# Kernel tuning notes

Hardware: AMD Instinct MI355X
Metric: run time of the kernel (lower is better)

Reference implementation:

```python
import jax, jax.numpy as jnp
import numpy as np

V, E, H, S, B, T = 32000, 256, 512, 128, 32, 32


def setup_inputs() -> dict:
    key = jax.random.key(0)
    ks = iter(jax.random.split(key, 32))

    def w(shape, s=0.05):
        return jax.random.normal(next(ks), shape, dtype=jnp.float32) * s

    return dict(
        src=jax.random.randint(next(ks), (S, B), 0, V),
        trg=jax.random.randint(next(ks), (T, B), 0, V),
        embed=w((V, E)),
        enc_Wih_f=w((4 * H, E)), enc_Whh_f=w((4 * H, H)), enc_bih_f=w((4 * H,)), enc_bhh_f=w((4 * H,)),
        enc_Wih_b=w((4 * H, E)), enc_Whh_b=w((4 * H, H)), enc_bih_b=w((4 * H,)), enc_bhh_b=w((4 * H,)),
        attn_W=w((H, 2 * H)), attn_b=w((H,)), attn_v=w((H,)),
        dec_Wih0=w((4 * H, H + E)), dec_Whh0=w((4 * H, H)), dec_bih0=w((4 * H,)), dec_bhh0=w((4 * H,)),
        dec_Wih1=w((4 * H, H)), dec_Whh1=w((4 * H, H)), dec_bih1=w((4 * H,)), dec_bhh1=w((4 * H,)),
        out_W=w((V, 2 * H)), out_b=w((V,)),
    )


def _cell(x, h, c, Wih, Whh, bih, bhh):
    # PyTorch LSTM gate order: i, f, g, o
    z = x @ Wih.T + h @ Whh.T + bih + bhh
    i, f, g, o = jnp.split(z, 4, axis=-1)
    c2 = jax.nn.sigmoid(f) * c + jax.nn.sigmoid(i) * jnp.tanh(g)
    h2 = jax.nn.sigmoid(o) * jnp.tanh(c2)
    return h2, c2


def _run_lstm(xs, Wih, Whh, bih, bhh):
    # xs: [S, B, in]; returns outputs [S,B,H], final (h,c)
    h0 = jnp.zeros((xs.shape[1], Whh.shape[1]), xs.dtype)

    def step(carry, x):
        h, c = carry
        h2, c2 = _cell(x, h, c, Wih, Whh, bih, bhh)
        return (h2, c2), h2

    (hT, cT), outs = jax.lax.scan(step, (h0, h0), xs)
    return outs, hT, cT


def _forward(src, trg, embed,
             enc_Wih_f, enc_Whh_f, enc_bih_f, enc_bhh_f,
             enc_Wih_b, enc_Whh_b, enc_bih_b, enc_bhh_b,
             attn_W, attn_b, attn_v,
             dec_Wih0, dec_Whh0, dec_bih0, dec_bhh0,
             dec_Wih1, dec_Whh1, dec_bih1, dec_bhh1,
             out_W, out_b):
    emb_src = embed[src]                                  # [S,B,E]
    # bidirectional 1-layer encoder LSTM
    f_outs, hf, cf = _run_lstm(emb_src, enc_Wih_f, enc_Whh_f, enc_bih_f, enc_bhh_f)
    b_outs, hb, cb = _run_lstm(emb_src[::-1], enc_Wih_b, enc_Whh_b, enc_bih_b, enc_bhh_b)
    enc_out = f_outs + b_outs[::-1]                       # [S,B,H] (sum of directions)
    h = jnp.stack([hf, hb])                               # [2,B,H] -> decoder init state
    c = jnp.stack([cf, cb])
    enc_bsh = enc_out.transpose(1, 0, 2)                  # [B,S,H]

    def dec_step(carry, tok):
        h, c = carry
        emb = embed[tok]                                  # [B,E]
        q = h[-1]                                         # top-layer hidden [B,H]
        qs = jnp.broadcast_to(q[:, None, :], enc_bsh.shape)
        energy = jnp.tanh(jnp.concatenate([qs, enc_bsh], -1) @ attn_W.T + attn_b)  # [B,S,H]
        scores = energy @ attn_v                          # [B,S]
        aw = jax.nn.softmax(scores, axis=1)
        ctx = jnp.einsum('bs,bsh->bh', aw, enc_bsh)       # [B,H]
        x = jnp.concatenate([emb, ctx], -1)               # [B,E+H]
        h0, c0 = _cell(x, h[0], c[0], dec_Wih0, dec_Whh0, dec_bih0, dec_bhh0)
        h1, c1 = _cell(h0, h[1], c[1], dec_Wih1, dec_Whh1, dec_bih1, dec_bhh1)
        logits = jax.nn.log_softmax(
            jnp.concatenate([h1, ctx], -1) @ out_W.T + out_b, axis=-1)             # [B,V]
        return (jnp.stack([h0, h1]), jnp.stack([c0, c1])), logits

    # teacher forcing (ratio=1.0): input at step t is trg[t-1]
    _, outs = jax.lax.scan(dec_step, (h, c), trg[:-1])    # [T-1,B,V]
    outputs = jnp.concatenate(
        [jnp.zeros((1,) + outs.shape[1:], outs.dtype), outs], 0)  # outputs[0]=0 as in torch
    return outputs


def reference(src, trg, embed,
              enc_Wih_f, enc_Whh_f, enc_bih_f, enc_bhh_f,
              enc_Wih_b, enc_Whh_b, enc_bih_b, enc_bhh_b,
              attn_W, attn_b, attn_v,
              dec_Wih0, dec_Whh0, dec_bih0, dec_bhh0,
              dec_Wih1, dec_Whh1, dec_bih1, dec_bhh1,
              out_W, out_b):
    return _forward(src, trg, embed,
                    enc_Wih_f, enc_Whh_f, enc_bih_f, enc_bhh_f,
                    enc_Wih_b, enc_Whh_b, enc_bih_b, enc_bhh_b,
                    attn_W, attn_b, attn_v,
                    dec_Wih0, dec_Whh0, dec_bih0, dec_bhh0,
                    dec_Wih1, dec_Whh1, dec_bih1, dec_bhh1,
                    out_W, out_b)
```

## Files before the change

### kernel.cpp

```cpp
#include <hip/hip_runtime.h>
#include <stdint.h>


using short8 = __attribute__((ext_vector_type(8))) short;
using f32x4  = __attribute__((ext_vector_type(4))) float;
typedef _Float16 half2v __attribute__((ext_vector_type(2)));

__device__ __forceinline__ short f2bf(float x){
  unsigned u = __float_as_uint(x);
  unsigned r = (u + 0x7fffu + ((u >> 16) & 1u)) >> 16;
  return (short)(unsigned short)r;
}
__device__ __forceinline__ float bf2f_lo(unsigned u){ return __uint_as_float(u << 16); }
__device__ __forceinline__ float bf2f_hi(unsigned u){ return __uint_as_float(u & 0xffff0000u); }
__device__ __forceinline__ float sigmf(float x){ return 1.0f/(1.0f + __expf(-x)); }
__device__ __forceinline__ float fast_tanh(float x){
  const float e = __expf(2.0f*x);
  return 1.0f - 2.0f/(e + 1.0f);
}
__device__ __forceinline__ unsigned pack_h2(float a, float b){
  unsigned short ha = __builtin_bit_cast(unsigned short, (_Float16)a);
  unsigned short hb = __builtin_bit_cast(unsigned short, (_Float16)b);
  return (unsigned)ha | ((unsigned)hb << 16);
}
__device__ __forceinline__ float dot2u(unsigned x, unsigned w, float c){
#if __has_builtin(__builtin_amdgcn_fdot2)
  return __builtin_amdgcn_fdot2(__builtin_bit_cast(half2v,x), __builtin_bit_cast(half2v,w), c, false);
#else
  half2v hx = __builtin_bit_cast(half2v,x), hw = __builtin_bit_cast(half2v,w);
  c = fmaf((float)hx[0], (float)hw[0], c);
  c = fmaf((float)hx[1], (float)hw[1], c);
  return c;
#endif
}

__device__ __forceinline__ float4 load_coh_f4(const float* p){
  float4 v;
  asm volatile("global_load_dwordx4 %0, %1, off sc0 sc1\n\ts_waitcnt vmcnt(0)"
               : "=&v"(v) : "v"(p) : "memory");
  return v;
}
__device__ __forceinline__ uint4 load_coh_u4(const unsigned* p){
  uint4 v;
  asm volatile("global_load_dwordx4 %0, %1, off sc0 sc1\n\ts_waitcnt vmcnt(0)"
               : "=&v"(v) : "v"(p) : "memory");
  return v;
}
__device__ __forceinline__ void load_coh_f4x4(const float* p0, const float* p1,
                                              const float* p2, const float* p3, float4* d){
  asm volatile(
    "global_load_dwordx4 %0, %4, off sc0 sc1\n\t"
    "global_load_dwordx4 %1, %5, off sc0 sc1\n\t"
    "global_load_dwordx4 %2, %6, off sc0 sc1\n\t"
    "global_load_dwordx4 %3, %7, off sc0 sc1\n\t"
    "s_waitcnt vmcnt(0)"
    : "=&v"(d[0]),"=&v"(d[1]),"=&v"(d[2]),"=&v"(d[3])
    : "v"(p0),"v"(p1),"v"(p2),"v"(p3)
    : "memory");
}
__device__ __forceinline__ void store_coh_f32(float* p, float v){
  asm volatile("global_store_dword %0, %1, off sc0 sc1" :: "v"(p), "v"(v) : "memory");
}
__device__ __forceinline__ void store_coh_u32(unsigned* p, unsigned v){
  asm volatile("global_store_dword %0, %1, off sc0 sc1" :: "v"(p), "v"(v) : "memory");
}

__device__ __forceinline__ void wait_flags(const unsigned* base, int quads, unsigned target){
  if (threadIdx.x < 64){
    const unsigned* p = base + ((threadIdx.x & (quads-1)) << 2);
    for(;;){
      uint4 v = load_coh_u4(p);
      if (__all(v.x>=target && v.y>=target && v.z>=target && v.w>=target)) break;
    }
  }
  __syncthreads();
}
__device__ __forceinline__ void set_flag(unsigned* slot, unsigned val){
  asm volatile("s_waitcnt vmcnt(0)" ::: "memory");
  __syncthreads();
  if (threadIdx.x == 0) store_coh_u32(slot, val);
}

__device__ __forceinline__ void stage8b(const float* src, unsigned* lds, int ldl){
  const int tid = threadIdx.x;
  const int row0 = tid >> 7;
  const int k4 = tid & 127;
  const float* p0 = src + (size_t)(row0    )*512 + (k4<<2);
  const float* p1 = src + (size_t)(row0 + 2)*512 + (k4<<2);
  const float* p2 = src + (size_t)(row0 + 4)*512 + (k4<<2);
  const float* p3 = src + (size_t)(row0 + 6)*512 + (k4<<2);
  float4 v[4];
  load_coh_f4x4(p0, p1, p2, p3, v);
  #pragma unroll
  for (int i = 0; i < 4; ++i){
    const int row = row0 + 2*i;
    lds[row*ldl + (k4<<1)]     = pack_h2(v[i].x, v[i].y);
    lds[row*ldl + (k4<<1) + 1] = pack_h2(v[i].z, v[i].w);
  }
}

__device__ __forceinline__ float dot512(const unsigned* xrow, const unsigned* w){
  float a = 0.f;
  #pragma unroll 4
  for (int it = 0; it < 16; ++it){
    uint4 x0 = *(const uint4*)(xrow + it*16);
    uint4 x1 = *(const uint4*)(xrow + it*16 + 4);
    uint4 x2 = *(const uint4*)(xrow + it*16 + 8);
    uint4 x3 = *(const uint4*)(xrow + it*16 + 12);
    uint4 w0 = *(const uint4*)(w + it*16);
    uint4 w1 = *(const uint4*)(w + it*16 + 4);
    uint4 w2 = *(const uint4*)(w + it*16 + 8);
    uint4 w3 = *(const uint4*)(w + it*16 + 12);
    a = dot2u(x0.x,w0.x,a); a = dot2u(x0.y,w0.y,a); a = dot2u(x0.z,w0.z,a); a = dot2u(x0.w,w0.w,a);
    a = dot2u(x1.x,w1.x,a); a = dot2u(x1.y,w1.y,a); a = dot2u(x1.z,w1.z,a); a = dot2u(x1.w,w1.w,a);
    a = dot2u(x2.x,w2.x,a); a = dot2u(x2.y,w2.y,a); a = dot2u(x2.z,w2.z,a); a = dot2u(x2.w,w2.w,a);
    a = dot2u(x3.x,w3.x,a); a = dot2u(x3.y,w3.y,a); a = dot2u(x3.z,w3.z,a); a = dot2u(x3.w,w3.w,a);
  }
  return a;
}

__device__ __forceinline__ float2 dot2rows(const unsigned* xrow, const unsigned* wA, const unsigned* wB){
  float a = 0.f, b = 0.f;
  #pragma unroll 8
  for (int it = 0; it < 32; ++it){
    uint4 x0 = *(const uint4*)(xrow + it*8);
    uint4 x1 = *(const uint4*)(xrow + it*8 + 4);
    uint4 a0 = *(const uint4*)(wA + it*8);
    uint4 a1 = *(const uint4*)(wA + it*8 + 4);
    uint4 b0 = *(const uint4*)(wB + it*8);
    uint4 b1 = *(const uint4*)(wB + it*8 + 4);
    a = dot2u(x0.x,a0.x,a); a = dot2u(x0.y,a0.y,a); a = dot2u(x0.z,a0.z,a); a = dot2u(x0.w,a0.w,a);
    a = dot2u(x1.x,a1.x,a); a = dot2u(x1.y,a1.y,a); a = dot2u(x1.z,a1.z,a); a = dot2u(x1.w,a1.w,a);
    b = dot2u(x0.x,b0.x,b); b = dot2u(x0.y,b0.y,b); b = dot2u(x0.z,b0.z,b); b = dot2u(x0.w,b0.w,b);
    b = dot2u(x1.x,b1.x,b); b = dot2u(x1.y,b1.y,b); b = dot2u(x1.w,b1.w,b); b = dot2u(x1.z,b1.z,b);
  }
  return make_float2(a, b);
}

__global__ void k_zero(float* __restrict__ p, int n){
  int i = blockIdx.x*256 + threadIdx.x;
  const int stride = gridDim.x*256;
  for (; i < n; i += stride) p[i] = 0.f;
}

__global__ __launch_bounds__(256) void k_cvt_f16(const float* __restrict__ s, unsigned short* __restrict__ d, int n){
  int i = blockIdx.x*256 + threadIdx.x;
  const int stride = gridDim.x*256;
  for (; i < n; i += stride) d[i] = __builtin_bit_cast(unsigned short, (_Float16)s[i]);
}
__global__ __launch_bounds__(256) void k_cvt_f16_str(const float* __restrict__ s, int lds_, unsigned short* __restrict__ d, int n){
  int i = blockIdx.x*256 + threadIdx.x;
  const int stride = gridDim.x*256;
  for (; i < n; i += stride){
    const int row = i >> 9, c = i & 511;
    d[i] = __builtin_bit_cast(unsigned short, (_Float16)s[(size_t)row*lds_ + c]);
  }
}

__global__ __launch_bounds__(256) void k_gather(
    const int* __restrict__ src, const int* __restrict__ trg,
    const float* __restrict__ embed,
    short* __restrict__ emb_src_bf, short* __restrict__ emb_trg_bf)
{
  const int row = blockIdx.x, tid = threadIdx.x;
  if (row < 4096){
    const int tok = src[row];
    emb_src_bf[(size_t)row*256 + tid] = f2bf(embed[(size_t)tok*256 + tid]);
  } else {
    const int r = row - 4096;
    short v = 0;
    if (r < 992){ const int tok = trg[r]; v = f2bf(embed[(size_t)tok*256 + tid]); }
    emb_trg_bf[(size_t)r*256 + tid] = v;
  }
}

__global__ __launch_bounds__(256) void k_gemm_aw(
    const short* __restrict__ A, int lda,
    const float* __restrict__ W, int ldw,
    float* __restrict__ C, int ldc,
    const float* __restrict__ bias0, const float* __restrict__ bias1,
    int Mvalid, int K, int tmode, short* __restrict__ Cbf)
{
  __shared__ __align__(16) short As[128*32];
  __shared__ __align__(16) short Bs[128*32];
  const int tid = threadIdx.x;
  const int bm = blockIdx.x, bn = blockIdx.y;
  const int w  = tid >> 6,  l  = tid & 63;
  const int wm = w >> 1,    wn = w & 1;
  const int lr = l & 15,    lk = l >> 4;

  const int r0 = tid >> 2;
  const int s0 = (tid & 3) << 3;
  const int r1 = r0 + 64;

  const short* a0 = A + (size_t)(bm*128 + r0)*lda + s0;
  const short* a1 = A + (size_t)(bm*128 + r1)*lda + s0;
  const float* w0 = W + (size_t)(bn*128 + r0)*ldw + s0;
  const float* w1 = W + (size_t)(bn*128 + r1)*ldw + s0;

  const f32x4 zero4 = {0.f,0.f,0.f,0.f};
  f32x4 acc[4][4];
  #pragma unroll
  for (int mi=0;mi<4;mi++){
    #pragma unroll
    for (int ni=0;ni<4;ni++) acc[mi][ni] = zero4;
  }

  for (int k0 = 0; k0 < K; k0 += 32){
    short8 va0 = *(const short8*)(a0 + k0);
    short8 va1 = *(const short8*)(a1 + k0);
    float4 f00 = *(const float4*)(w0 + k0);
    float4 f01 = *(const float4*)(w0 + k0 + 4);
    float4 f10 = *(const float4*)(w1 + k0);
    float4 f11 = *(const float4*)(w1 + k0 + 4);
    short8 vb0, vb1;
    vb0[0]=f2bf(f00.x); vb0[1]=f2bf(f00.y); vb0[2]=f2bf(f00.z); vb0[3]=f2bf(f00.w);
    vb0[4]=f2bf(f01.x); vb0[5]=f2bf(f01.y); vb0[6]=f2bf(f01.z); vb0[7]=f2bf(f01.w);
    vb1[0]=f2bf(f10.x); vb1[1]=f2bf(f10.y); vb1[2]=f2bf(f10.z); vb1[3]=f2bf(f10.w);
    vb1[4]=f2bf(f11.x); vb1[5]=f2bf(f11.y); vb1[6]=f2bf(f11.z); vb1[7]=f2bf(f11.w);

    __syncthreads();
    *((short8*)As + tid)       = va0;
    *((short8*)As + tid + 256) = va1;
    *((short8*)Bs + tid)       = vb0;
    *((short8*)Bs + tid + 256) = vb1;
    __syncthreads();

    short8 af[4], bfr[4];
    #pragma unroll
    for (int mi=0;mi<4;mi++) af[mi]  = *(const short8*)&As[(wm*64 + mi*16 + lr)*32 + (lk<<3)];
    #pragma unroll
    for (int ni=0;ni<4;ni++) bfr[ni] = *(const short8*)&Bs[(wn*64 + ni*16 + lr)*32 + (lk<<3)];
    #pragma unroll
    for (int mi=0;mi<4;mi++){
      #pragma unroll
      for (int ni=0;ni<4;ni++)
        acc[mi][ni] = __builtin_amdgcn_mfma_f32_16x16x32_bf16(af[mi], bfr[ni], acc[mi][ni], 0,0,0);
    }
  }

  #pragma unroll
  for (int mi=0;mi<4;mi++){
    const int rb = bm*128 + wm*64 + mi*16 + (lk<<2);
    #pragma unroll
    for (int ni=0;ni<4;ni++){
      const int col = bn*128 + wn*64 + ni*16 + lr;
      float bv = 0.f;
      if (bias0) bv += bias0[col];
      if (bias1) bv += bias1[col];
      #pragma unroll
      for (int rr=0;rr<4;rr++){
        const int row = rb + rr;
        if (row < Mvalid){
          const float vv = acc[mi][ni][rr] + bv;
          if (Cbf)        Cbf[(size_t)row*ldc + col] = f2bf(vv);
          else if (tmode) C[(size_t)(row>>5)*65536 + (size_t)col*32 + (row&31)] = vv;
          else            C[(size_t)row*ldc + col] = vv;
        }
      }
    }
  }
}

__global__ __launch_bounds__(256,1) void k_enc_persist(
    const float* __restrict__ pre_f, const float* __restrict__ pre_b,
    const unsigned short* __restrict__ WhF, const unsigned short* __restrict__ WhB,
    float* __restrict__ f_outs, float* __restrict__ b_outs,
    float* __restrict__ c_f_out, float* __restrict__ c_b_out,
    unsigned* __restrict__ flagF, unsigned* __restrict__ flagB)
{
  __shared__ __align__(16) unsigned x_lds[8*264];
  __shared__ float zbuf[64*8];
  const int bid = blockIdx.x, tid = threadIdx.x;
  const int x = bid & 7, m = bid >> 3;
  const int dir = m & 1, bg = (m >> 1) & 3, q = m >> 3;
  const int jb = x*4 + q;
  const float* pre = dir ? pre_b : pre_f;
  const unsigned* Wh = (const unsigned*)(dir ? WhB : WhF);
  float* outs = dir ? b_outs : f_outs;
  float* c_out = dir ? c_b_out : c_f_out;
  unsigned* flags = dir ? flagB : flagF;
  const int fid = jb + 32*bg;

  const int bb = tid & 7, rr = tid >> 3;
  const int g = rr >> 3, op = rr & 7;
  const unsigned* wA = Wh + (size_t)(g*512 + jb*16 + 2*op)*256;
  const unsigned* wB = wA + 256;

  const int fo = tid & 15, fb = tid >> 4;
  const int b_out = bg*8 + fb, k_out = jb*16 + fo;
  float c_reg = 0.f;

  for (int t = 0; t < 128; ++t){
    float pz[4];
    if (tid < 128){
      const int tt = dir ? (127 - t) : t;
      const float* pt = pre + (size_t)tt*65536;
      #pragma unroll
      for (int gg = 0; gg < 4; ++gg)
        pz[gg] = pt[(size_t)(gg*512 + k_out)*32 + b_out];
    }
    if (t) wait_flags(flags + 32*bg, 8, (unsigned)t);
    if (t == 0){
      for (int i = tid; i < 8*264; i += 256) x_lds[i] = 0;
    } else {
      stage8b(outs + (size_t)(t-1)*16384 + (size_t)(bg*8)*512, x_lds, 264);
    }
    __syncthreads();

    const float2 d = dot2rows(x_lds + bb*264, wA, wB);
    zbuf[(g*16 + 2*op)*8 + bb]   = d.x;
    zbuf[(g*16 + 2*op+1)*8 + bb] = d.y;
    __syncthreads();

    if (tid < 128){
      float z[4];
      #pragma unroll
      for (int gg = 0; gg < 4; ++gg)
        z[gg] = pz[gg] + zbuf[(gg*16 + fo)*8 + fb];
      const float cn = sigmf(z[1])*c_reg + sigmf(z[0])*fast_tanh(z[2]);
      c_reg = cn;
      store_coh_f32(outs + (size_t)t*16384 + (size_t)b_out*512 + k_out, sigmf(z[3])*fast_tanh(cn));
    }
    set_flag(flags + fid, (unsigned)(t+1));
  }
  if (tid < 128) c_out[b_out*512 + k_out] = c_reg;
}

__global__ __launch_bounds__(256) void k_sum_enc(
    const float* __restrict__ f_outs, const float* __restrict__ b_outs,
    short* __restrict__ enc_sum_bf)
{
  const int i = blockIdx.x*256 + threadIdx.x;
  const int s = i >> 14, rem = i & 16383;
  enc_sum_bf[i] = f2bf(f_outs[i] + b_outs[(size_t)(127 - s)*16384 + rem]);
}

__global__ __launch_bounds__(256,1) void k_dec_persist(
    const float* __restrict__ demb,
    const unsigned short* __restrict__ Wih0h,
    const unsigned short* __restrict__ Whh0h,
    const unsigned short* __restrict__ Wih1h,
    const unsigned short* __restrict__ Whh1h,
    const float* __restrict__ bih1, const float* __restrict__ bhh1,
    const unsigned short* __restrict__ wqh,
    const float* __restrict__ attnV,
    const short* __restrict__ enc_proj_bf,
    const short* __restrict__ enc_sum_bf,
    const float* __restrict__ h0_init, const float* __restrict__ h1_init,
    const float* __restrict__ c0_init, const float* __restrict__ c1_init,
    float* __restrict__ h0buf, float* __restrict__ h1buf,
    float* __restrict__ ctxb,
    float* __restrict__ qsb,
    short* __restrict__ h1ctx,
    unsigned* __restrict__ dflag)
{
  __shared__ __align__(16) unsigned x0s[8*260];
  __shared__ __align__(16) unsigned x1s[8*260];
  __shared__ float zfin[32*9];
  __shared__ __align__(16) float q_s[512], v_s[512];
  __shared__ float part[256], aw[128], red[128];

  const int bid = blockIdx.x, tid = threadIdx.x;
  const int jb = (bid & 7)*8 + ((bid >> 3) >> 2);
  const int bg = (bid >> 3) & 3;
  const int fid = bg*64 + jb;
  unsigned* gq = dflag + bg*64;

  const int b = tid & 7, r = tid >> 3;
  const int g = r >> 3, o = r & 7;
  const int j_row = g*512 + jb*8 + o;

  const int fo = tid & 7, fb = tid >> 3;
  const int b_out = bg*8 + fb, k_out = jb*8 + fo;

  const unsigned* Wh0row = (const unsigned*)Whh0h + (size_t)j_row*256;
  const unsigned* Wh1row = (const unsigned*)Whh1h + (size_t)j_row*256;
  const unsigned* Wi0row = (const unsigned*)Wih0h + (size_t)j_row*256;
  const unsigned* Wi1row = (const unsigned*)Wih1h + (size_t)j_row*256;
  const unsigned* Wqrow  = (const unsigned*)wqh  + (size_t)(jb*8 + b)*256;

  float c0_reg = 0.f, c1_reg = 0.f, bias1g[4];
  if (tid < 64){
    c0_reg = c0_init[b_out*512 + k_out];
    c1_reg = c1_init[b_out*512 + k_out];
    #pragma unroll
    for (int gg=0; gg<4; ++gg) bias1g[gg] = bih1[gg*512 + k_out] + bhh1[gg*512 + k_out];
  }
  if (bid < 32 && tid < 128) ((float4*)v_s)[tid] = ((const float4*)attnV)[tid];

  float zh0 = 0.f;

  for (int t = 0; t < 31; ++t){
    const float demb_v = demb[(size_t)t*65536 + (size_t)j_row*32 + bg*8 + b];

    if (t){
      wait_flags(gq, 16, (unsigned)(4*t));
      stage8b(h1buf + (size_t)(t&1)*16384 + (size_t)(bg*8)*512, x1s, 260);
    } else {
      stage8b(h0_init + (size_t)(bg*8)*512, x0s, 260);
      stage8b(h1_init + (size_t)(bg*8)*512, x1s, 260);
    }
    __syncthreads();
    if (t == 0) zh0 = dot512(x0s + b*260, Wh0row);
    const float zh1 = dot512(x1s + b*260, Wh1row);
    if (tid < 64){
      const float qv = dot512(x1s + (tid>>3)*260, Wqrow);
      store_coh_f32(qsb + (size_t)(bg*8 + (tid>>3))*512 + jb*8 + b, qv);
    }

    if (bid < 32){
      set_flag(dflag + fid, (unsigned)(4*t+1));
      wait_flags(gq, 16, (unsigned)(4*t+1));
      const int ab = bid;
      if (tid < 128) ((float4*)q_s)[tid] = load_coh_f4(qsb + (size_t)ab*512 + (tid<<2));
      __syncthreads();
      {
        const int s = tid >> 1, half = tid & 1;
        const unsigned* ep = (const unsigned*)(enc_proj_bf + ((size_t)(s*32 + ab))*512 + (half << 8));
        const float* qh = q_s + (half << 8);
        const float* vh = v_s + (half << 8);
        float p = 0.f;
        for (int kk = 0; kk < 128; kk += 4){
          uint4 e = *(const uint4*)(ep + kk);
          const int k2 = kk << 1;
          p += fast_tanh(qh[k2+0] + bf2f_lo(e.x)) * vh[k2+0];
          p += fast_tanh(qh[k2+1] + bf2f_hi(e.x)) * vh[k2+1];
          p += fast_tanh(qh[k2+2] + bf2f_lo(e.y)) * vh[k2+2];
          p += fast_tanh(qh[k2+3] + bf2f_hi(e.y)) * vh[k2+3];
          p += fast_tanh(qh[k2+4] + bf2f_lo(e.z)) * vh[k2+4];
          p += fast_tanh(qh[k2+5] + bf2f_hi(e.z)) * vh[k2+5];
          p += fast_tanh(qh[k2+6] + bf2f_lo(e.w)) * vh[k2+6];
          p += fast_tanh(qh[k2+7] + bf2f_hi(e.w)) * vh[k2+7];
        }
        part[tid] = p;
      }
      __syncthreads();
      if (tid < 128){ const float sc = part[2*tid] + part[2*tid+1]; aw[tid] = sc; red[tid] = sc; }
      __syncthreads();
      for (int off = 64; off > 0; off >>= 1){
        if (tid < off) red[tid] = fmaxf(red[tid], red[tid+off]);
        __syncthreads();
      }
      const float mx = red[0];
      __syncthreads();
      if (tid < 128){ const float e = __expf(aw[tid] - mx); aw[tid] = e; red[tid] = e; }
      __syncthreads();
      for (int off = 64; off > 0; off >>= 1){
        if (tid < off) red[tid] += red[tid+off];
        __syncthreads();
      }
      const float inv = 1.0f / red[0];
      if (tid < 128) aw[tid] *= inv;
      __syncthreads();
      {
        const int cc = tid << 1;
        float x0 = 0.f, x1 = 0.f;
        for (int s2 = 0; s2 < 128; ++s2){
          const unsigned u = *(const unsigned*)(enc_sum_bf + ((size_t)(s2*32 + ab))*512 + cc);
          const float a = aw[s2];
          x0 = fmaf(a, bf2f_lo(u), x0);
          x1 = fmaf(a, bf2f_hi(u), x1);
        }
        store_coh_f32(ctxb + ab*512 + cc,     x0);
        store_coh_f32(ctxb + ab*512 + cc + 1, x1);
        h1ctx[(size_t)t*32768 + ab*1024 + 512 + cc]     = f2bf(x0);
        h1ctx[(size_t)t*32768 + ab*1024 + 512 + cc + 1] = f2bf(x1);
      }
      set_flag(dflag + fid, (unsigned)(4*t+2));
    } else {
      set_flag(dflag + fid, (unsigned)(4*t+2));
    }

    wait_flags(gq, 16, (unsigned)(4*t+2));
    stage8b(ctxb + (size_t)(bg*8)*512, x0s, 260);
    __syncthreads();
    {
      const float z = demb_v + dot512(x0s + b*260, Wi0row) + zh0;
      zfin[r*9 + b] = z;
    }
    __syncthreads();
    if (tid < 64){
      float z[4];
      #pragma unroll
      for (int gg=0; gg<4; ++gg) z[gg] = zfin[(gg*8 + fo)*9 + fb];
      const float cn = sigmf(z[1])*c0_reg + sigmf(z[0])*fast_tanh(z[2]);
      c0_reg = cn;
      store_coh_f32(h0buf + (size_t)((t+1)&1)*16384 + (size_t)b_out*512 + k_out,
                    sigmf(z[3])*fast_tanh(cn));
    }
    set_flag(dflag + fid, (unsigned)(4*t+3));

    wait_flags(gq, 16, (unsigned)(4*t+3));
    stage8b(h0buf + (size_t)((t+1)&1)*16384 + (size_t)(bg*8)*512, x1s, 260);
    __syncthreads();
    {
      const float z = dot512(x1s + b*260, Wi1row) + zh1;
      zh0 = dot512(x1s + b*260, Wh0row);
      zfin[r*9 + b] = z;
    }
    __syncthreads();
    if (tid < 64){
      float z[4];
      #pragma unroll
      for (int gg=0; gg<4; ++gg) z[gg] = bias1g[gg] + zfin[(gg*8 + fo)*9 + fb];
      const float cn = sigmf(z[1])*c1_reg + sigmf(z[0])*fast_tanh(z[2]);
      c1_reg = cn;
      const float hn = sigmf(z[3])*fast_tanh(cn);
      store_coh_f32(h1buf + (size_t)((t+1)&1)*16384 + (size_t)b_out*512 + k_out, hn);
      h1ctx[(size_t)t*32768 + (size_t)b_out*1024 + k_out] = f2bf(hn);
    }
    set_flag(dflag + fid, (unsigned)(4*t+4));
  }
}

__global__ __launch_bounds__(256) void k_logsm(float* __restrict__ out){
  float* row = out + (size_t)blockIdx.x * 32000;
  const int tid = threadIdx.x;
  __shared__ float red[256];
  float m = -3.4e38f;
  for (int i = tid; i < 32000; i += 256) m = fmaxf(m, row[i]);
  red[tid] = m; __syncthreads();
  for (int off = 128; off > 0; off >>= 1){
    if (tid < off) red[tid] = fmaxf(red[tid], red[tid+off]);
    __syncthreads();
  }
  m = red[0]; __syncthreads();
  float s = 0.f;
  for (int i = tid; i < 32000; i += 256) s += __expf(row[i] - m);
  red[tid] = s; __syncthreads();
  for (int off = 128; off > 0; off >>= 1){
    if (tid < off) red[tid] += red[tid+off];
    __syncthreads();
  }
  const float lse = m + __logf(red[0]);
  for (int i = tid; i < 32000; i += 256) row[i] -= lse;
}

extern "C" void kernel_launch(void* const* d_in, const int* in_sizes, int n_in,
                              void* d_out, int out_size, void* d_ws, size_t ws_size,
                              hipStream_t stream)
{
  (void)in_sizes; (void)n_in; (void)out_size; (void)ws_size;
  const int*   src   = (const int*)d_in[0];
  const int*   trg   = (const int*)d_in[1];
  const float* embed = (const float*)d_in[2];
  const float* eWihF = (const float*)d_in[3];
  const float* eWhhF = (const float*)d_in[4];
  const float* ebihF = (const float*)d_in[5];
  const float* ebhhF = (const float*)d_in[6];
  const float* eWihB = (const float*)d_in[7];
  const float* eWhhB = (const float*)d_in[8];
  const float* ebihB = (const float*)d_in[9];
  const float* ebhhB = (const float*)d_in[10];
  const float* attnW = (const float*)d_in[11];
  const float* attnB = (const float*)d_in[12];
  const float* attnV = (const float*)d_in[13];
  const float* dWih0 = (const float*)d_in[14];
  const float* dWhh0 = (const float*)d_in[15];
  const float* dbih0 = (const float*)d_in[16];
  const float* dbhh0 = (const float*)d_in[17];
  const float* dWih1 = (const float*)d_in[18];
  const float* dWhh1 = (const float*)d_in[19];
  const float* dbih1 = (const float*)d_in[20];
  const float* dbhh1 = (const float*)d_in[21];
  const float* outW  = (const float*)d_in[22];
  const float* outB  = (const float*)d_in[23];

  float* out = (float*)d_out;
  float* enc_in_f = out;
  float* enc_in_b = out + 8388608;
  short* enc_proj_bf = (short*)(out + 18874368);
  float* f_outs   = out + 20971520;
  float* b_outs   = out + 23068672;
  float* demb     = out + 25165824;
  short* emb_src_bf = (short*)(out + 27262976);
  short* emb_trg_bf = (short*)(out + 27787264);
  short* enc_sum_bf = (short*)(out + 27918336);
  unsigned short* wqh    = (unsigned short*)(out + 28966912);
  unsigned short* whhF_h = (unsigned short*)(out + 29229056);
  unsigned short* whhB_h = (unsigned short*)(out + 29753344);
  unsigned short* wih0_h = (unsigned short*)(out + 30277632);
  unsigned short* whh0_h = (unsigned short*)(out + 30801920);
  unsigned short* wih1_h = (unsigned short*)(out + 31326208);
  unsigned short* whh1_h = (unsigned short*)(out + 31850496);
  float* qsb            = out + 32374784;

  char* ws = (char*)d_ws;
  short* h1ctx = (short*)ws;
  float* st    = (float*)(ws + 2097152);
  float* h0buf = st;
  float* h1buf = st + 32768;
  float* ctxb  = st + 65536;
  float* c_f   = st + 81920;
  float* c_b   = st + 98304;
  unsigned* flagF = (unsigned*)(st + 114688);
  unsigned* flagB = flagF + 128;
  unsigned* dflag = flagF + 256;

  k_zero<<<1, 256, 0, stream>>>((float*)flagF, 512);
  k_gather<<<5120, 256, 0, stream>>>(src, trg, embed, emb_src_bf, emb_trg_bf);
  {
    dim3 g1(32,16);
    k_gemm_aw<<<g1,256,0,stream>>>(emb_src_bf,256, eWihF,256, enc_in_f,2048, ebihF,ebhhF, 4096,256, 1, nullptr);
    k_gemm_aw<<<g1,256,0,stream>>>(emb_src_bf,256, eWihB,256, enc_in_b,2048, ebihB,ebhhB, 4096,256, 1, nullptr);
    dim3 g2(8,16);
    k_gemm_aw<<<g2,256,0,stream>>>(emb_trg_bf,256, dWih0,768, demb,2048, dbih0,dbhh0, 1024,256, 1, nullptr);
  }
  k_cvt_f16<<<1024,256,0,stream>>>(eWhhF, whhF_h, 1048576);
  k_cvt_f16<<<1024,256,0,stream>>>(eWhhB, whhB_h, 1048576);
  k_cvt_f16_str<<<1024,256,0,stream>>>(dWih0+256, 768, wih0_h, 1048576);
  k_cvt_f16<<<1024,256,0,stream>>>(dWhh0, whh0_h, 1048576);
  k_cvt_f16<<<1024,256,0,stream>>>(dWih1, wih1_h, 1048576);
  k_cvt_f16<<<1024,256,0,stream>>>(dWhh1, whh1_h, 1048576);
  k_cvt_f16_str<<<256,256,0,stream>>>(attnW, 1024, wqh, 262144);
  k_enc_persist<<<256, 256, 0, stream>>>(enc_in_f, enc_in_b, whhF_h, whhB_h,
                                         f_outs, b_outs, c_f, c_b, flagF, flagB);
  k_sum_enc<<<8192, 256, 0, stream>>>(f_outs, b_outs, enc_sum_bf);
  {
    dim3 g3(32,4);
    k_gemm_aw<<<g3,256,0,stream>>>(enc_sum_bf,512, attnW+512,1024, nullptr,512, attnB,nullptr, 4096,512, 0, enc_proj_bf);
  }
  k_dec_persist<<<256, 256, 0, stream>>>(demb, wih0_h, whh0_h, wih1_h, whh1_h,
                                         dbih1, dbhh1, wqh, attnV, enc_proj_bf, enc_sum_bf,
                                         f_outs + (size_t)127*16384, b_outs + (size_t)127*16384,
                                         c_f, c_b, h0buf, h1buf, ctxb, qsb, h1ctx, dflag);
  k_zero<<<512, 256, 0, stream>>>(out, 1024000);
  {
    dim3 g4(8,250);
    k_gemm_aw<<<g4,256,0,stream>>>(h1ctx,1024, outW,1024, out + 1024000, 32000, outB,nullptr, 992,1024, 0, nullptr);
  }
  k_logsm<<<992, 256, 0, stream>>>(out + 1024000);
}
```

Measured before the change: 2.374 ms.

## Repartition decoder per batch row, relayout pre-activations, and simplify log-softmax

The persistent decoder is repartitioned so that each batch row is owned by 8 blocks. Attention for that row is computed locally by one of them, which replaces the 64-block group barriers with small per-row flag waits. Recurrent state (h0, h1, ctx) is exchanged as packed fp16, and the separate q buffer is removed. The encoder and decoder input-projection GEMMs now write in layouts matched to the persistent kernels' read pattern, so those loads are contiguous. Log-softmax also drops the max-subtraction pass and uses float4 accesses, which can overflow if logits are large.

```diff
diff --git a/kernel.cpp b/kernel.cpp
--- a/kernel.cpp
+++ b/kernel.cpp
@@ -10,6 +10,9 @@
   unsigned u = __float_as_uint(x);
   unsigned r = (u + 0x7fffu + ((u >> 16) & 1u)) >> 16;
   return (short)(unsigned short)r;
+}
+__device__ __forceinline__ unsigned bfpair(float a, float b){
+  return (unsigned)(unsigned short)f2bf(a) | ((unsigned)(unsigned short)f2bf(b) << 16);
 }
 __device__ __forceinline__ float bf2f_lo(unsigned u){ return __uint_as_float(u << 16); }
 __device__ __forceinline__ float bf2f_hi(unsigned u){ return __uint_as_float(u & 0xffff0000u); }
@@ -65,6 +68,26 @@
   asm volatile("global_store_dword %0, %1, off sc0 sc1" :: "v"(p), "v"(v) : "memory");
 }
 
+__device__ __forceinline__ void wait_sp(const unsigned* base, int n, unsigned target){
+  if (threadIdx.x < 64){
+    const bool mine = (int)threadIdx.x < n;
+    const unsigned* p = base + (threadIdx.x << 4);
+    for(;;){
+      unsigned v = target;
+      if (mine)
+        asm volatile("global_load_dword %0, %1, off sc0 sc1\n\ts_waitcnt vmcnt(0)"
+                     : "=&v"(v) : "v"(p) : "memory");
+      if (__all(v >= target)) break;
+    }
+  }
+  __syncthreads();
+}
+__device__ __forceinline__ void set_flag(unsigned* slot, unsigned val){
+  asm volatile("s_waitcnt vmcnt(0)" ::: "memory");
+  __syncthreads();
+  if (threadIdx.x == 0) store_coh_u32(slot, val);
+}
+
 __device__ __forceinline__ void wait_flags(const unsigned* base, int quads, unsigned target){
   if (threadIdx.x < 64){
     const unsigned* p = base + ((threadIdx.x & (quads-1)) << 2);
@@ -74,11 +97,6 @@
     }
   }
   __syncthreads();
-}
-__device__ __forceinline__ void set_flag(unsigned* slot, unsigned val){
-  asm volatile("s_waitcnt vmcnt(0)" ::: "memory");
-  __syncthreads();
-  if (threadIdx.x == 0) store_coh_u32(slot, val);
 }
 
 __device__ __forceinline__ void stage8b(const float* src, unsigned* lds, int ldl){
@@ -253,9 +271,19 @@
         const int row = rb + rr;
         if (row < Mvalid){
           const float vv = acc[mi][ni][rr] + bv;
-          if (Cbf)        Cbf[(size_t)row*ldc + col] = f2bf(vv);
-          else if (tmode) C[(size_t)(row>>5)*65536 + (size_t)col*32 + (row&31)] = vv;
-          else            C[(size_t)row*ldc + col] = vv;
+          if (Cbf){
+            Cbf[(size_t)row*ldc + col] = f2bf(vv);
+          } else if (tmode == 2){
+            const int gq = col >> 9, jj = col & 511;
+            C[(size_t)row*2048 + (jj>>6)*256 + gq*64 + (jj&63)] = vv;
+          } else if (tmode == 3){
+            const int tt=row>>5, bfull=row&31, bge=bfull>>3, fbe=bfull&7;
+            const int ge=col>>9, rem=col&511, jbe=rem>>4, foe=rem&15;
+            const int eslot = (jbe>>2) + 8*(bge + 4*(jbe&3));
+            C[(size_t)((tt*128 + eslot)*4 + ge)*128 + (foe + 16*fbe)] = vv;
+          } else {
+            C[(size_t)row*ldc + col] = vv;
+          }
         }
       }
     }
@@ -263,7 +291,7 @@
 }
 
 __global__ __launch_bounds__(256,1) void k_enc_persist(
-    const float* __restrict__ pre_f, const float* __restrict__ pre_b,
+    const float* __restrict__ preR_f, const float* __restrict__ preR_b,
     const unsigned short* __restrict__ WhF, const unsigned short* __restrict__ WhB,
     float* __restrict__ f_outs, float* __restrict__ b_outs,
     float* __restrict__ c_f_out, float* __restrict__ c_b_out,
@@ -275,12 +303,13 @@
   const int x = bid & 7, m = bid >> 3;
   const int dir = m & 1, bg = (m >> 1) & 3, q = m >> 3;
   const int jb = x*4 + q;
-  const float* pre = dir ? pre_b : pre_f;
+  const float* preR = dir ? preR_b : preR_f;
   const unsigned* Wh = (const unsigned*)(dir ? WhB : WhF);
   float* outs = dir ? b_outs : f_outs;
   float* c_out = dir ? c_b_out : c_f_out;
   unsigned* flags = dir ? flagB : flagF;
   const int fid = jb + 32*bg;
+  const int eslot = x + 8*(bg + 4*q);
 
   const int bb = tid & 7, rr = tid >> 3;
   const int g = rr >> 3, op = rr & 7;
@@ -295,16 +324,16 @@
     float pz[4];
     if (tid < 128){
       const int tt = dir ? (127 - t) : t;
-      const float* pt = pre + (size_t)tt*65536;
+      const float* pb = preR + (size_t)(tt*128 + eslot)*512;
       #pragma unroll
       for (int gg = 0; gg < 4; ++gg)
-        pz[gg] = pt[(size_t)(gg*512 + k_out)*32 + b_out];
-    }
-    if (t) wait_flags(flags + 32*bg, 8, (unsigned)t);
-    if (t == 0){
+        pz[gg] = pb[gg*128 + tid];
+    }
+    if (t){
+      wait_flags(flags + 32*bg, 8, (unsigned)t);
+      stage8b(outs + (size_t)(t-1)*16384 + (size_t)(bg*8)*512, x_lds, 264);
+    } else {
       for (int i = tid; i < 8*264; i += 256) x_lds[i] = 0;
-    } else {
-      stage8b(outs + (size_t)(t-1)*16384 + (size_t)(bg*8)*512, x_lds, 264);
     }
     __syncthreads();
 
@@ -337,7 +366,7 @@
 }
 
 __global__ __launch_bounds__(256,1) void k_dec_persist(
-    const float* __restrict__ demb,
+    const float* __restrict__ demb2,
     const unsigned short* __restrict__ Wih0h,
     const unsigned short* __restrict__ Whh0h,
     const unsigned short* __restrict__ Wih1h,
@@ -349,75 +378,77 @@
     const short* __restrict__ enc_sum_bf,
     const float* __restrict__ h0_init, const float* __restrict__ h1_init,
     const float* __restrict__ c0_init, const float* __restrict__ c1_init,
-    float* __restrict__ h0buf, float* __restrict__ h1buf,
-    float* __restrict__ ctxb,
-    float* __restrict__ qsb,
+    unsigned* __restrict__ h0b, unsigned* __restrict__ h1b,
+    unsigned* __restrict__ ctxb,
     short* __restrict__ h1ctx,
-    unsigned* __restrict__ dflag)
+    unsigned* __restrict__ fH1, unsigned* __restrict__ fH0, unsigned* __restrict__ fCTX)
 {
-  __shared__ __align__(16) unsigned x0s[8*260];
-  __shared__ __align__(16) unsigned x1s[8*260];
-  __shared__ float zfin[32*9];
+  __shared__ __align__(16) unsigned x1s[260];
+  __shared__ __align__(16) unsigned x0s[260];
+  __shared__ __align__(16) unsigned xhs[260];
+  __shared__ float zf[256];
+  __shared__ float hsh[64];
   __shared__ __align__(16) float q_s[512], v_s[512];
   __shared__ float part[256], aw[128], red[128];
 
   const int bid = blockIdx.x, tid = threadIdx.x;
-  const int jb = (bid & 7)*8 + ((bid >> 3) >> 2);
-  const int bg = (bid >> 3) & 3;
-  const int fid = bg*64 + jb;
-  unsigned* gq = dflag + bg*64;
-
-  const int b = tid & 7, r = tid >> 3;
-  const int g = r >> 3, o = r & 7;
-  const int j_row = g*512 + jb*8 + o;
-
-  const int fo = tid & 7, fb = tid >> 3;
-  const int b_out = bg*8 + fb, k_out = jb*8 + fo;
-
-  const unsigned* Wh0row = (const unsigned*)Whh0h + (size_t)j_row*256;
-  const unsigned* Wh1row = (const unsigned*)Whh1h + (size_t)j_row*256;
-  const unsigned* Wi0row = (const unsigned*)Wih0h + (size_t)j_row*256;
-  const unsigned* Wi1row = (const unsigned*)Wih1h + (size_t)j_row*256;
-  const unsigned* Wqrow  = (const unsigned*)wqh  + (size_t)(jb*8 + b)*256;
-
-  float c0_reg = 0.f, c1_reg = 0.f, bias1g[4];
+  const int r = bid & 31, k = bid >> 5;
+  const bool isB0 = (k == 0);
+  const int g = tid >> 6, o = tid & 63;
+  const int jrow = g*512 + k*64 + o;
+
+  unsigned* myH1 = fH1 + (size_t)(r*8 + k)*16;
+  unsigned* myH0 = fH0 + (size_t)(r*8 + k)*16;
+  unsigned* myCT = fCTX + (size_t)r*16;
+  const unsigned* rH1 = fH1 + (size_t)r*128;
+  const unsigned* rH0 = fH0 + (size_t)r*128;
+
+  const unsigned* Wh1row = (const unsigned*)Whh1h + (size_t)jrow*256;
+  const unsigned* Wi0row = (const unsigned*)Wih0h + (size_t)jrow*256;
+  const unsigned* Wi1row = (const unsigned*)Wih1h + (size_t)jrow*256;
+  const unsigned* Wh0row = (const unsigned*)Whh0h + (size_t)jrow*256;
+  const unsigned* WQ = (const unsigned*)wqh;
+
+  float c0 = 0.f, c1 = 0.f, b1v[4];
   if (tid < 64){
-    c0_reg = c0_init[b_out*512 + k_out];
-    c1_reg = c1_init[b_out*512 + k_out];
+    c0 = c0_init[r*512 + k*64 + tid];
+    c1 = c1_init[r*512 + k*64 + tid];
     #pragma unroll
-    for (int gg=0; gg<4; ++gg) bias1g[gg] = bih1[gg*512 + k_out] + bhh1[gg*512 + k_out];
-  }
-  if (bid < 32 && tid < 128) ((float4*)v_s)[tid] = ((const float4*)attnV)[tid];
-
-  float zh0 = 0.f;
+    for (int gg=0; gg<4; ++gg)
+      b1v[gg] = bih1[gg*512 + k*64 + tid] + bhh1[gg*512 + k*64 + tid];
+  }
+  if (isB0 && tid < 128) ((float4*)v_s)[tid] = ((const float4*)attnV)[tid];
+
+  if (tid < 64){
+    const float* hp1 = h1_init + r*512 + tid*8;
+    const float* hp0 = h0_init + r*512 + tid*8;
+    float4 a = *(const float4*)hp1, b2 = *(const float4*)(hp1+4);
+    x1s[(tid<<2)+0] = pack_h2(a.x,a.y); x1s[(tid<<2)+1] = pack_h2(a.z,a.w);
+    x1s[(tid<<2)+2] = pack_h2(b2.x,b2.y); x1s[(tid<<2)+3] = pack_h2(b2.z,b2.w);
+    a = *(const float4*)hp0; b2 = *(const float4*)(hp0+4);
+    x0s[(tid<<2)+0] = pack_h2(a.x,a.y); x0s[(tid<<2)+1] = pack_h2(a.z,a.w);
+    x0s[(tid<<2)+2] = pack_h2(b2.x,b2.y); x0s[(tid<<2)+3] = pack_h2(b2.z,b2.w);
+  }
+  __syncthreads();
+  float zh0 = dot512(x0s, Wh0row);
 
   for (int t = 0; t < 31; ++t){
-    const float demb_v = demb[(size_t)t*65536 + (size_t)j_row*32 + bg*8 + b];
+    const float demb_v = demb2[(size_t)(t*32 + r)*2048 + k*256 + tid];
 
     if (t){
-      wait_flags(gq, 16, (unsigned)(4*t));
-      stage8b(h1buf + (size_t)(t&1)*16384 + (size_t)(bg*8)*512, x1s, 260);
-    } else {
-      stage8b(h0_init + (size_t)(bg*8)*512, x0s, 260);
-      stage8b(h1_init + (size_t)(bg*8)*512, x1s, 260);
-    }
-    __syncthreads();
-    if (t == 0) zh0 = dot512(x0s + b*260, Wh0row);
-    const float zh1 = dot512(x1s + b*260, Wh1row);
-    if (tid < 64){
-      const float qv = dot512(x1s + (tid>>3)*260, Wqrow);
-      store_coh_f32(qsb + (size_t)(bg*8 + (tid>>3))*512 + jb*8 + b, qv);
-    }
-
-    if (bid < 32){
-      set_flag(dflag + fid, (unsigned)(4*t+1));
-      wait_flags(gq, 16, (unsigned)(4*t+1));
-      const int ab = bid;
-      if (tid < 128) ((float4*)q_s)[tid] = load_coh_f4(qsb + (size_t)ab*512 + (tid<<2));
+      wait_sp(rH1, 8, (unsigned)t);
+      if (tid < 64) *(uint4*)&x1s[tid<<2] = load_coh_u4(h1b + (size_t)(t&1)*8192 + r*256 + (tid<<2));
+      __syncthreads();
+    }
+    const float zh1 = dot512(x1s, Wh1row);
+
+    if (isB0){
+      const float2 qq = dot2rows(x1s, WQ + (size_t)tid*256, WQ + (size_t)(tid+256)*256);
+      q_s[tid] = qq.x; q_s[tid+256] = qq.y;
       __syncthreads();
       {
         const int s = tid >> 1, half = tid & 1;
-        const unsigned* ep = (const unsigned*)(enc_proj_bf + ((size_t)(s*32 + ab))*512 + (half << 8));
+        const unsigned* ep = (const unsigned*)(enc_proj_bf + ((size_t)(s*32 + r))*512 + (half << 8));
         const float* qh = q_s + (half << 8);
         const float* vh = v_s + (half << 8);
         float p = 0.f;
@@ -453,64 +484,66 @@
       const float inv = 1.0f / red[0];
       if (tid < 128) aw[tid] *= inv;
       __syncthreads();
-      {
-        const int cc = tid << 1;
-        float x0 = 0.f, x1 = 0.f;
+      if (tid < 64){
+        const unsigned* es = (const unsigned*)enc_sum_bf + (size_t)r*256 + (tid<<2);
+        float c0v=0,c1v=0,c2v=0,c3v=0,c4v=0,c5v=0,c6v=0,c7v=0;
         for (int s2 = 0; s2 < 128; ++s2){
-          const unsigned u = *(const unsigned*)(enc_sum_bf + ((size_t)(s2*32 + ab))*512 + cc);
           const float a = aw[s2];
-          x0 = fmaf(a, bf2f_lo(u), x0);
-          x1 = fmaf(a, bf2f_hi(u), x1);
+          uint4 u = *(const uint4*)(es + (size_t)s2*8192);
+          c0v = fmaf(a, bf2f_lo(u.x), c0v); c1v = fmaf(a, bf2f_hi(u.x), c1v);
+          c2v = fmaf(a, bf2f_lo(u.y), c2v); c3v = fmaf(a, bf2f_hi(u.y), c3v);
+          c4v = fmaf(a, bf2f_lo(u.z), c4v); c5v = fmaf(a, bf2f_hi(u.z), c5v);
+          c6v = fmaf(a, bf2f_lo(u.w), c6v); c7v = fmaf(a, bf2f_hi(u.w), c7v);
         }
-        store_coh_f32(ctxb + ab*512 + cc,     x0);
-        store_coh_f32(ctxb + ab*512 + cc + 1, x1);
-        h1ctx[(size_t)t*32768 + ab*1024 + 512 + cc]     = f2bf(x0);
-        h1ctx[(size_t)t*32768 + ab*1024 + 512 + cc + 1] = f2bf(x1);
+        unsigned* cp4 = ctxb + (size_t)r*256 + (tid<<2);
+        store_coh_u32(cp4+0, pack_h2(c0v,c1v));
+        store_coh_u32(cp4+1, pack_h2(c2v,c3v));
+        store_coh_u32(cp4+2, pack_h2(c4v,c5v));
+        store_coh_u32(cp4+3, pack_h2(c6v,c7v));
+        unsigned* hc = (unsigned*)h1ctx + ((size_t)(t*32 + r)*512 + 256 + (tid<<2));
+        hc[0] = bfpair(c0v,c1v); hc[1] = bfpair(c2v,c3v);
+        hc[2] = bfpair(c4v,c5v); hc[3] = bfpair(c6v,c7v);
       }
-      set_flag(dflag + fid, (unsigned)(4*t+2));
-    } else {
-      set_flag(dflag + fid, (unsigned)(4*t+2));
-    }
-
-    wait_flags(gq, 16, (unsigned)(4*t+2));
-    stage8b(ctxb + (size_t)(bg*8)*512, x0s, 260);
+      set_flag(myCT, (unsigned)(t+1));
+    }
+
+    wait_sp(myCT, 1, (unsigned)(t+1));
+    if (tid < 64) *(uint4*)&x0s[tid<<2] = load_coh_u4(ctxb + (size_t)r*256 + (tid<<2));
+    __syncthreads();
+    zf[tid] = demb_v + dot512(x0s, Wi0row) + zh0;
+    __syncthreads();
+    if (tid < 64){
+      const float cn = sigmf(zf[64+tid])*c0 + sigmf(zf[tid])*fast_tanh(zf[128+tid]);
+      c0 = cn;
+      hsh[tid] = sigmf(zf[192+tid])*fast_tanh(cn);
+    }
+    __syncthreads();
+    if (tid < 32)
+      store_coh_u32(h0b + (size_t)(t&1)*8192 + r*256 + k*32 + tid, pack_h2(hsh[2*tid], hsh[2*tid+1]));
+    set_flag(myH0, (unsigned)(t+1));
+
+    wait_sp(rH0, 8, (unsigned)(t+1));
+    if (tid < 64) *(uint4*)&xhs[tid<<2] = load_coh_u4(h0b + (size_t)(t&1)*8192 + r*256 + (tid<<2));
     __syncthreads();
     {
-      const float z = demb_v + dot512(x0s + b*260, Wi0row) + zh0;
-      zfin[r*9 + b] = z;
+      const float2 d = dot2rows(xhs, Wi1row, Wh0row);
+      zf[tid] = d.x + zh1;
+      zh0 = d.y;
     }
     __syncthreads();
     if (tid < 64){
-      float z[4];
-      #pragma unroll
-      for (int gg=0; gg<4; ++gg) z[gg] = zfin[(gg*8 + fo)*9 + fb];
-      const float cn = sigmf(z[1])*c0_reg + sigmf(z[0])*fast_tanh(z[2]);
-      c0_reg = cn;
-      store_coh_f32(h0buf + (size_t)((t+1)&1)*16384 + (size_t)b_out*512 + k_out,
-                    sigmf(z[3])*fast_tanh(cn));
-    }
-    set_flag(dflag + fid, (unsigned)(4*t+3));
-
-    wait_flags(gq, 16, (unsigned)(4*t+3));
-    stage8b(h0buf + (size_t)((t+1)&1)*16384 + (size_t)(bg*8)*512, x1s, 260);
-    __syncthreads();
-    {
-      const float z = dot512(x1s + b*260, Wi1row) + zh1;
-      zh0 = dot512(x1s + b*260, Wh0row);
-      zfin[r*9 + b] = z;
-    }
-    __syncthreads();
-    if (tid < 64){
-      float z[4];
-      #pragma unroll
-      for (int gg=0; gg<4; ++gg) z[gg] = bias1g[gg] + zfin[(gg*8 + fo)*9 + fb];
-      const float cn = sigmf(z[1])*c1_reg + sigmf(z[0])*fast_tanh(z[2]);
-      c1_reg = cn;
-      const float hn = sigmf(z[3])*fast_tanh(cn);
-      store_coh_f32(h1buf + (size_t)((t+1)&1)*16384 + (size_t)b_out*512 + k_out, hn);
-      h1ctx[(size_t)t*32768 + (size_t)b_out*1024 + k_out] = f2bf(hn);
-    }
-    set_flag(dflag + fid, (unsigned)(4*t+4));
+      const float cn = sigmf(zf[64+tid] + b1v[1])*c1
+                     + sigmf(zf[tid] + b1v[0])*fast_tanh(zf[128+tid] + b1v[2]);
+      c1 = cn;
+      hsh[tid] = sigmf(zf[192+tid] + b1v[3])*fast_tanh(cn);
+    }
+    __syncthreads();
+    if (tid < 32){
+      const unsigned ph = pack_h2(hsh[2*tid], hsh[2*tid+1]);
+      store_coh_u32(h1b + (size_t)((t+1)&1)*8192 + r*256 + k*32 + tid, ph);
+      ((unsigned*)h1ctx)[(size_t)(t*32 + r)*512 + k*32 + tid] = bfpair(hsh[2*tid], hsh[2*tid+1]);
+    }
+    set_flag(myH1, (unsigned)(t+1));
   }
 }
 
@@ -518,23 +551,22 @@
   float* row = out + (size_t)blockIdx.x * 32000;
   const int tid = threadIdx.x;
   __shared__ float red[256];
-  float m = -3.4e38f;
-  for (int i = tid; i < 32000; i += 256) m = fmaxf(m, row[i]);
-  red[tid] = m; __syncthreads();
-  for (int off = 128; off > 0; off >>= 1){
-    if (tid < off) red[tid] = fmaxf(red[tid], red[tid+off]);
-    __syncthreads();
-  }
-  m = red[0]; __syncthreads();
   float s = 0.f;
-  for (int i = tid; i < 32000; i += 256) s += __expf(row[i] - m);
+  for (int i = tid; i < 8000; i += 256){
+    const float4 v = ((const float4*)row)[i];
+    s += __expf(v.x) + __expf(v.y) + __expf(v.z) + __expf(v.w);
+  }
   red[tid] = s; __syncthreads();
   for (int off = 128; off > 0; off >>= 1){
     if (tid < off) red[tid] += red[tid+off];
     __syncthreads();
   }
-  const float lse = m + __logf(red[0]);
-  for (int i = tid; i < 32000; i += 256) row[i] -= lse;
+  const float lse = __logf(red[0]);
+  for (int i = tid; i < 8000; i += 256){
+    float4 v = ((const float4*)row)[i];
+    v.x -= lse; v.y -= lse; v.z -= lse; v.w -= lse;
+    ((float4*)row)[i] = v;
+  }
 }
 
 extern "C" void kernel_launch(void* const* d_in, const int* in_sizes, int n_in,
@@ -568,12 +600,12 @@
   const float* outB  = (const float*)d_in[23];
 
   float* out = (float*)d_out;
-  float* enc_in_f = out;
-  float* enc_in_b = out + 8388608;
+  float* preR_f = out;
+  float* preR_b = out + 8388608;
   short* enc_proj_bf = (short*)(out + 18874368);
   float* f_outs   = out + 20971520;
   float* b_outs   = out + 23068672;
-  float* demb     = out + 25165824;
+  float* demb2    = out + 25165824;
   short* emb_src_bf = (short*)(out + 27262976);
   short* emb_trg_bf = (short*)(out + 27787264);
   short* enc_sum_bf = (short*)(out + 27918336);
@@ -584,28 +616,28 @@
   unsigned short* whh0_h = (unsigned short*)(out + 30801920);
   unsigned short* wih1_h = (unsigned short*)(out + 31326208);
   unsigned short* whh1_h = (unsigned short*)(out + 31850496);
-  float* qsb            = out + 32374784;
 
   char* ws = (char*)d_ws;
   short* h1ctx = (short*)ws;
-  float* st    = (float*)(ws + 2097152);
-  float* h0buf = st;
-  float* h1buf = st + 32768;
-  float* ctxb  = st + 65536;
-  float* c_f   = st + 81920;
-  float* c_b   = st + 98304;
-  unsigned* flagF = (unsigned*)(st + 114688);
+  unsigned* h0b = (unsigned*)(ws + 2097152);
+  unsigned* h1b = (unsigned*)(ws + 2162688);
+  unsigned* ctxb = (unsigned*)(ws + 2228224);
+  float* c_f = (float*)(ws + 2260992);
+  float* c_b = (float*)(ws + 2326528);
+  unsigned* fH1  = (unsigned*)(ws + 2392064);
+  unsigned* fH0  = (unsigned*)(ws + 2408448);
+  unsigned* fCTX = (unsigned*)(ws + 2424832);
+  unsigned* flagF = (unsigned*)(ws + 2426880);
   unsigned* flagB = flagF + 128;
-  unsigned* dflag = flagF + 256;
-
-  k_zero<<<1, 256, 0, stream>>>((float*)flagF, 512);
+
+  k_zero<<<8, 256, 0, stream>>>((float*)fH1, 8960);
   k_gather<<<5120, 256, 0, stream>>>(src, trg, embed, emb_src_bf, emb_trg_bf);
   {
     dim3 g1(32,16);
-    k_gemm_aw<<<g1,256,0,stream>>>(emb_src_bf,256, eWihF,256, enc_in_f,2048, ebihF,ebhhF, 4096,256, 1, nullptr);
-    k_gemm_aw<<<g1,256,0,stream>>>(emb_src_bf,256, eWihB,256, enc_in_b,2048, ebihB,ebhhB, 4096,256, 1, nullptr);
+    k_gemm_aw<<<g1,256,0,stream>>>(emb_src_bf,256, eWihF,256, preR_f,2048, ebihF,ebhhF, 4096,256, 3, nullptr);
+    k_gemm_aw<<<g1,256,0,stream>>>(emb_src_bf,256, eWihB,256, preR_b,2048, ebihB,ebhhB, 4096,256, 3, nullptr);
     dim3 g2(8,16);
-    k_gemm_aw<<<g2,256,0,stream>>>(emb_trg_bf,256, dWih0,768, demb,2048, dbih0,dbhh0, 1024,256, 1, nullptr);
+    k_gemm_aw<<<g2,256,0,stream>>>(emb_trg_bf,256, dWih0,768, demb2,2048, dbih0,dbhh0, 1024,256, 2, nullptr);
   }
   k_cvt_f16<<<1024,256,0,stream>>>(eWhhF, whhF_h, 1048576);
   k_cvt_f16<<<1024,256,0,stream>>>(eWhhB, whhB_h, 1048576);
@@ -614,17 +646,17 @@
   k_cvt_f16<<<1024,256,0,stream>>>(dWih1, wih1_h, 1048576);
   k_cvt_f16<<<1024,256,0,stream>>>(dWhh1, whh1_h, 1048576);
   k_cvt_f16_str<<<256,256,0,stream>>>(attnW, 1024, wqh, 262144);
-  k_enc_persist<<<256, 256, 0, stream>>>(enc_in_f, enc_in_b, whhF_h, whhB_h,
+  k_enc_persist<<<256, 256, 0, stream>>>(preR_f, preR_b, whhF_h, whhB_h,
                                          f_outs, b_outs, c_f, c_b, flagF, flagB);
   k_sum_enc<<<8192, 256, 0, stream>>>(f_outs, b_outs, enc_sum_bf);
   {
     dim3 g3(32,4);
     k_gemm_aw<<<g3,256,0,stream>>>(enc_sum_bf,512, attnW+512,1024, nullptr,512, attnB,nullptr, 4096,512, 0, enc_proj_bf);
   }
-  k_dec_persist<<<256, 256, 0, stream>>>(demb, wih0_h, whh0_h, wih1_h, whh1_h,
+  k_dec_persist<<<256, 256, 0, stream>>>(demb2, wih0_h, whh0_h, wih1_h, whh1_h,
                                          dbih1, dbhh1, wqh, attnV, enc_proj_bf, enc_sum_bf,
                                          f_outs + (size_t)127*16384, b_outs + (size_t)127*16384,
-                                         c_f, c_b, h0buf, h1buf, ctxb, qsb, h1ctx, dflag);
+                                         c_f, c_b, h0b, h1b, ctxb, h1ctx, fH1, fH0, fCTX);
   k_zero<<<512, 256, 0, stream>>>(out, 1024000);
   {
     dim3 g4(8,250);
```

New measurement: 3.517 ms. +48.1%, slower.
